# Optimization experiments

Hardware: AMD Instinct MI355X
Metric: run time of the kernel (lower is better)

The kernel has to match this reference:

```python
import jax, jax.numpy as jnp
import numpy as np

KSIZE = 3  # module init kwarg


def setup_inputs() -> dict:
    key = jax.random.key(0)
    k1, k2, k3 = jax.random.split(key, 3)
    shape = (16, 3, 512, 512)  # [B, C, H, W]
    return {
        "sr": jax.random.normal(k1, shape, jnp.float32),
        "sr_ema": jax.random.normal(k2, shape, jnp.float32),
        "hr": jax.random.normal(k3, shape, jnp.float32),
    }


def _local_var(res, ksize):
    """Unbiased variance over a ksize x ksize sliding window with reflect pad.

    Matches torch: reflect-pad then unfold + var(unbiased=True). Implemented as a
    box-filter over sum and sum-of-squares (no ksize^2-larger unfold tensor).
    res: [B, 1, H, W] -> [B, 1, H, W]
    """
    pad = (ksize - 1) // 2
    rp = jnp.pad(res, ((0, 0), (0, 0), (pad, pad), (pad, pad)), mode="reflect")
    n = ksize * ksize
    win = (1, 1, ksize, ksize)
    strides = (1, 1, 1, 1)
    zero = jnp.zeros((), rp.dtype)
    s = jax.lax.reduce_window(rp, zero, jax.lax.add, win, strides, "VALID")
    sq = jax.lax.reduce_window(rp * rp, zero, jax.lax.add, win, strides, "VALID")
    # unbiased: (sum(x^2) - sum(x)^2/n) / (n-1)
    return (sq - s * s / n) / (n - 1)


def reference(sr, sr_ema, hr):
    # per-pixel channel-summed residuals, [B, 1, H, W]
    residual_ema = jnp.sum(jnp.abs(hr - sr_ema), axis=1, keepdims=True) / 255.0
    residual_sr = jnp.sum(jnp.abs(hr - sr), axis=1, keepdims=True) / 255.0

    r_det = jax.lax.stop_gradient(residual_sr)  # .clone().detach() in torch

    # patch-level weight: unbiased var over (C=1, H, W) per sample, ** (1/5)
    n_patch = r_det.shape[1] * r_det.shape[2] * r_det.shape[3]
    mean = jnp.mean(r_det, axis=(-1, -2, -3), keepdims=True)
    patch_var = jnp.sum((r_det - mean) ** 2, axis=(-1, -2, -3), keepdims=True) / (n_patch - 1)
    patch_w = patch_var ** 0.2  # [B,1,1,1]

    pixel_w = _local_var(r_det, KSIZE)  # [B,1,H,W]

    overall_w = patch_w * pixel_w
    overall_w = jnp.where(residual_sr < residual_ema, jnp.zeros((), overall_w.dtype), overall_w)

    # L1 loss (mean reduction) between weighted sr and weighted hr
    return jnp.mean(jnp.abs(overall_w * sr - overall_w * hr))
```

## Files before the change

### kernel.cpp

```cpp
#include <hip/hip_runtime.h>
#include <math.h>


#define BB 16
#define HH 512
#define WW 512
#define HW (HH * WW)
#define CHW (3 * HW)
#define TILES_PER_BATCH 64
#define NBLOCKS (BB * TILES_PER_BATCH)
#define LDS_STRIDE 264

__device__ __forceinline__ int reflect_h(int gh) {
  gh = gh < 0 ? -gh : gh;
  return gh >= HH ? 2 * HH - 2 - gh : gh;
}

__global__ __launch_bounds__(256) void wl1_main(
    const float* __restrict__ sr, const float* __restrict__ srema,
    const float* __restrict__ hr,
    float* __restrict__ p_sum, float* __restrict__ p_sum2,
    float* __restrict__ p_loss) {
  __shared__ float rt[18][LDS_STRIDE];
  const int bid = blockIdx.x;
  const int b = bid >> 6;
  const int t = bid & 63;
  const int h0 = (t >> 1) << 4;
  const int w0 = (t & 1) << 8;
  const int tid = threadIdx.x;
  const int c4 = tid & 63;
  const int rs = tid >> 6;
  const float* __restrict__ srb = sr + (size_t)b * CHW;
  const float* __restrict__ hrb = hr + (size_t)b * CHW;
  const float* __restrict__ eb = srema + (size_t)b * CHW;

#pragma unroll
  for (int it = 0; it < 5; ++it) {
    int row = it * 4 + rs;
    if (row < 18) {
      int gh = reflect_h(h0 - 1 + row);
      const float* hb = hrb + gh * WW + w0 + 4 * c4;
      const float* sb = srb + gh * WW + w0 + 4 * c4;
      float4 ha = *(const float4*)(hb);
      float4 hbv = *(const float4*)(hb + HW);
      float4 hc = *(const float4*)(hb + 2 * HW);
      float4 sa = *(const float4*)(sb);
      float4 sbv = *(const float4*)(sb + HW);
      float4 sc = *(const float4*)(sb + 2 * HW);
      float4 r4;
      r4.x = (fabsf(ha.x - sa.x) + fabsf(hbv.x - sbv.x) + fabsf(hc.x - sc.x)) / 255.0f;
      r4.y = (fabsf(ha.y - sa.y) + fabsf(hbv.y - sbv.y) + fabsf(hc.y - sc.y)) / 255.0f;
      r4.z = (fabsf(ha.z - sa.z) + fabsf(hbv.z - sbv.z) + fabsf(hc.z - sc.z)) / 255.0f;
      r4.w = (fabsf(ha.w - sa.w) + fabsf(hbv.w - sbv.w) + fabsf(hc.w - sc.w)) / 255.0f;
      *(float4*)&rt[row][4 + 4 * c4] = r4;
    }
  }
  if (tid < 36) {
    int row = tid >> 1, side = tid & 1;
    int gh = reflect_h(h0 - 1 + row);
    int gw = side ? w0 + 256 : w0 - 1;
    if (gw < 0) gw = 1;
    if (gw > 511) gw = 1022 - gw;
    int base = gh * WW + gw;
    float v = (fabsf(hrb[base] - srb[base]) +
               fabsf(hrb[base + HW] - srb[base + HW]) +
               fabsf(hrb[base + 2 * HW] - srb[base + 2 * HW])) /
              255.0f;
    rt[row][side ? 260 : 3] = v;
  }
  __syncthreads();

  float v1 = 0.f, v2 = 0.f, v3 = 0.f;
  const int row0 = rs * 4;
#pragma unroll
  for (int rr = 0; rr < 4; ++rr) {
    const int orow = row0 + rr;
    float cs[6] = {0, 0, 0, 0, 0, 0}, cq[6] = {0, 0, 0, 0, 0, 0};
    float center[4];
#pragma unroll
    for (int dr = 0; dr < 3; ++dr) {
      const float* lp = &rt[orow + dr][4 * c4];
      float4 a = *(const float4*)(lp);
      float4 bq = *(const float4*)(lp + 4);
      float4 cq4 = *(const float4*)(lp + 8);
      float f3 = a.w, f4 = bq.x, f5 = bq.y, f6 = bq.z, f7 = bq.w, f8 = cq4.x;
      cs[0] += f3; cq[0] += f3 * f3;
      cs[1] += f4; cq[1] += f4 * f4;
      cs[2] += f5; cq[2] += f5 * f5;
      cs[3] += f6; cq[3] += f6 * f6;
      cs[4] += f7; cq[4] += f7 * f7;
      cs[5] += f8; cq[5] += f8 * f8;
      if (dr == 1) { center[0] = f4; center[1] = f5; center[2] = f6; center[3] = f7; }
    }
    const int gbase = (h0 + orow) * WW + w0 + 4 * c4;
    float4 ha = *(const float4*)(hrb + gbase);
    float4 hb2 = *(const float4*)(hrb + gbase + HW);
    float4 hc = *(const float4*)(hrb + gbase + 2 * HW);
    float4 ea = *(const float4*)(eb + gbase);
    float4 eb2 = *(const float4*)(eb + gbase + HW);
    float4 ec = *(const float4*)(eb + gbase + 2 * HW);
    float e4[4];
    e4[0] = (fabsf(ha.x - ea.x) + fabsf(hb2.x - eb2.x) + fabsf(hc.x - ec.x)) / 255.0f;
    e4[1] = (fabsf(ha.y - ea.y) + fabsf(hb2.y - eb2.y) + fabsf(hc.y - ec.y)) / 255.0f;
    e4[2] = (fabsf(ha.z - ea.z) + fabsf(hb2.z - eb2.z) + fabsf(hc.z - ec.z)) / 255.0f;
    e4[3] = (fabsf(ha.w - ea.w) + fabsf(hb2.w - eb2.w) + fabsf(hc.w - ec.w)) / 255.0f;
#pragma unroll
    for (int cc = 0; cc < 4; ++cc) {
      float s = cs[cc] + cs[cc + 1] + cs[cc + 2];
      float q = cq[cc] + cq[cc + 1] + cq[cc + 2];
      float pvar = (q - s * s / 9.0f) / 8.0f;
      float rc = center[cc];
      v1 += rc;
      v2 += rc * rc;
      if (rc >= e4[cc]) v3 += pvar * (255.0f * rc);
    }
  }

#pragma unroll
  for (int off = 32; off > 0; off >>= 1) {
    v1 += __shfl_down(v1, off, 64);
    v2 += __shfl_down(v2, off, 64);
    v3 += __shfl_down(v3, off, 64);
  }
  __shared__ float red[3][4];
  if (c4 == 0) {
    red[0][rs] = v1;
    red[1][rs] = v2;
    red[2][rs] = v3;
  }
  __syncthreads();
  if (tid == 0) {
    p_sum[bid] = red[0][0] + red[0][1] + red[0][2] + red[0][3];
    p_sum2[bid] = red[1][0] + red[1][1] + red[1][2] + red[1][3];
    p_loss[bid] = red[2][0] + red[2][1] + red[2][2] + red[2][3];
  }
}

__global__ __launch_bounds__(1024) void wl1_reduce(
    const float* __restrict__ p_sum, const float* __restrict__ p_sum2,
    const float* __restrict__ p_loss, float* __restrict__ out) {
  const int tid = threadIdx.x;
  const int b = tid >> 6, k = tid & 63;
  const int i = b * TILES_PER_BATCH + k;
  double s = (double)p_sum[i], s2 = (double)p_sum2[i], sl = (double)p_loss[i];
#pragma unroll
  for (int off = 32; off > 0; off >>= 1) {
    s += __shfl_down(s, off, 64);
    s2 += __shfl_down(s2, off, 64);
    sl += __shfl_down(sl, off, 64);
  }
  __shared__ double acc[BB];
  if (k == 0) {
    const double n = (double)HW;
    double var = (s2 - s * s / n) / (n - 1.0);
    acc[b] = pow(var, 0.2) * sl;
  }
  __syncthreads();
  if (tid == 0) {
    double tot = 0.0;
#pragma unroll
    for (int j = 0; j < BB; ++j) tot += acc[j];
    out[0] = (float)(tot / (double)((size_t)BB * CHW));
  }
}

extern "C" void kernel_launch(void* const* d_in, const int* in_sizes, int n_in,
                              void* d_out, int out_size, void* d_ws,
                              size_t ws_size, hipStream_t stream) {
  const float* sr = (const float*)d_in[0];
  const float* srema = (const float*)d_in[1];
  const float* hr = (const float*)d_in[2];
  float* out = (float*)d_out;

  float* p_sum = (float*)d_ws;
  float* p_sum2 = p_sum + NBLOCKS;
  float* p_loss = p_sum2 + NBLOCKS;

  wl1_main<<<NBLOCKS, 256, 0, stream>>>(sr, srema, hr, p_sum, p_sum2, p_loss);
  wl1_reduce<<<1, 1024, 0, stream>>>(p_sum, p_sum2, p_loss, out);
}
```

Baseline: 158.8 us.

## Halve tile width and compute EMA residual from staged hr loads

Tiles shrink from 256 to 128 columns, which doubles the block count and raises the occupancy hint to 8 blocks per CU. Each thread computes the sr_ema residual in the load phase, reusing the hr float4 values already fetched for the sr residual. This removes the second read of hr in the compute loop. The reduce kernel now folds two partials per thread to cover the 128 tiles per batch. The extra halo traffic from narrower tiles and the conditional register selection are the trade-offs.

After: 166.4 us. +4.8%, slower.

```diff
diff --git a/kernel.cpp b/kernel.cpp
--- a/kernel.cpp
+++ b/kernel.cpp
@@ -7,38 +7,42 @@
 #define WW 512
 #define HW (HH * WW)
 #define CHW (3 * HW)
-#define TILES_PER_BATCH 64
+#define TILE_W 128
+#define TILES_PER_BATCH 128
 #define NBLOCKS (BB * TILES_PER_BATCH)
-#define LDS_STRIDE 264
+#define LDS_STRIDE 136
 
 __device__ __forceinline__ int reflect_h(int gh) {
   gh = gh < 0 ? -gh : gh;
   return gh >= HH ? 2 * HH - 2 - gh : gh;
 }
 
-__global__ __launch_bounds__(256) void wl1_main(
+__global__ __launch_bounds__(256, 8) void wl1_main(
     const float* __restrict__ sr, const float* __restrict__ srema,
     const float* __restrict__ hr,
     float* __restrict__ p_sum, float* __restrict__ p_sum2,
     float* __restrict__ p_loss) {
   __shared__ float rt[18][LDS_STRIDE];
   const int bid = blockIdx.x;
-  const int b = bid >> 6;
-  const int t = bid & 63;
-  const int h0 = (t >> 1) << 4;
-  const int w0 = (t & 1) << 8;
+  const int b = bid >> 7;
+  const int t = bid & 127;
+  const int h0 = (t >> 2) << 4;
+  const int w0 = (t & 3) << 7;
   const int tid = threadIdx.x;
-  const int c4 = tid & 63;
-  const int rs = tid >> 6;
+  const int c4 = tid & 31;
+  const int rsub = tid >> 5;
+  const int ob = (rsub + 7) & 7;
   const float* __restrict__ srb = sr + (size_t)b * CHW;
   const float* __restrict__ hrb = hr + (size_t)b * CHW;
   const float* __restrict__ eb = srema + (size_t)b * CHW;
 
+  float e0[4] = {0.f, 0.f, 0.f, 0.f};
+  float e1[4] = {0.f, 0.f, 0.f, 0.f};
 #pragma unroll
-  for (int it = 0; it < 5; ++it) {
-    int row = it * 4 + rs;
+  for (int it = 0; it < 3; ++it) {
+    const int row = it * 8 + rsub;
     if (row < 18) {
-      int gh = reflect_h(h0 - 1 + row);
+      const int gh = reflect_h(h0 - 1 + row);
       const float* hb = hrb + gh * WW + w0 + 4 * c4;
       const float* sb = srb + gh * WW + w0 + 4 * c4;
       float4 ha = *(const float4*)(hb);
@@ -53,12 +57,28 @@
       r4.z = (fabsf(ha.z - sa.z) + fabsf(hbv.z - sbv.z) + fabsf(hc.z - sc.z)) / 255.0f;
       r4.w = (fabsf(ha.w - sa.w) + fabsf(hbv.w - sbv.w) + fabsf(hc.w - sc.w)) / 255.0f;
       *(float4*)&rt[row][4 + 4 * c4] = r4;
+      const int orow = row - 1;
+      if (orow >= 0 && orow < 16) {
+        const float* ep = eb + gh * WW + w0 + 4 * c4;
+        float4 ea = *(const float4*)(ep);
+        float4 eb2 = *(const float4*)(ep + HW);
+        float4 ec = *(const float4*)(ep + 2 * HW);
+        float ex = (fabsf(ha.x - ea.x) + fabsf(hbv.x - eb2.x) + fabsf(hc.x - ec.x)) / 255.0f;
+        float ey = (fabsf(ha.y - ea.y) + fabsf(hbv.y - eb2.y) + fabsf(hc.y - ec.y)) / 255.0f;
+        float ez = (fabsf(ha.z - ea.z) + fabsf(hbv.z - eb2.z) + fabsf(hc.z - ec.z)) / 255.0f;
+        float ew = (fabsf(ha.w - ea.w) + fabsf(hbv.w - eb2.w) + fabsf(hc.w - ec.w)) / 255.0f;
+        if (orow == ob) {
+          e0[0] = ex; e0[1] = ey; e0[2] = ez; e0[3] = ew;
+        } else {
+          e1[0] = ex; e1[1] = ey; e1[2] = ez; e1[3] = ew;
+        }
+      }
     }
   }
   if (tid < 36) {
     int row = tid >> 1, side = tid & 1;
     int gh = reflect_h(h0 - 1 + row);
-    int gw = side ? w0 + 256 : w0 - 1;
+    int gw = side ? w0 + TILE_W : w0 - 1;
     if (gw < 0) gw = 1;
     if (gw > 511) gw = 1022 - gw;
     int base = gh * WW + gw;
@@ -66,15 +86,14 @@
                fabsf(hrb[base + HW] - srb[base + HW]) +
                fabsf(hrb[base + 2 * HW] - srb[base + 2 * HW])) /
               255.0f;
-    rt[row][side ? 260 : 3] = v;
+    rt[row][side ? 4 + TILE_W : 3] = v;
   }
   __syncthreads();
 
   float v1 = 0.f, v2 = 0.f, v3 = 0.f;
-  const int row0 = rs * 4;
 #pragma unroll
-  for (int rr = 0; rr < 4; ++rr) {
-    const int orow = row0 + rr;
+  for (int rr = 0; rr < 2; ++rr) {
+    const int orow = ob + rr * 8;
     float cs[6] = {0, 0, 0, 0, 0, 0}, cq[6] = {0, 0, 0, 0, 0, 0};
     float center[4];
 #pragma unroll
@@ -92,18 +111,7 @@
       cs[5] += f8; cq[5] += f8 * f8;
       if (dr == 1) { center[0] = f4; center[1] = f5; center[2] = f6; center[3] = f7; }
     }
-    const int gbase = (h0 + orow) * WW + w0 + 4 * c4;
-    float4 ha = *(const float4*)(hrb + gbase);
-    float4 hb2 = *(const float4*)(hrb + gbase + HW);
-    float4 hc = *(const float4*)(hrb + gbase + 2 * HW);
-    float4 ea = *(const float4*)(eb + gbase);
-    float4 eb2 = *(const float4*)(eb + gbase + HW);
-    float4 ec = *(const float4*)(eb + gbase + 2 * HW);
-    float e4[4];
-    e4[0] = (fabsf(ha.x - ea.x) + fabsf(hb2.x - eb2.x) + fabsf(hc.x - ec.x)) / 255.0f;
-    e4[1] = (fabsf(ha.y - ea.y) + fabsf(hb2.y - eb2.y) + fabsf(hc.y - ec.y)) / 255.0f;
-    e4[2] = (fabsf(ha.z - ea.z) + fabsf(hb2.z - eb2.z) + fabsf(hc.z - ec.z)) / 255.0f;
-    e4[3] = (fabsf(ha.w - ea.w) + fabsf(hb2.w - eb2.w) + fabsf(hc.w - ec.w)) / 255.0f;
+    const float* e4 = rr ? e1 : e0;
 #pragma unroll
     for (int cc = 0; cc < 4; ++cc) {
       float s = cs[cc] + cs[cc + 1] + cs[cc + 2];
@@ -123,10 +131,11 @@
     v3 += __shfl_down(v3, off, 64);
   }
   __shared__ float red[3][4];
-  if (c4 == 0) {
-    red[0][rs] = v1;
-    red[1][rs] = v2;
-    red[2][rs] = v3;
+  const int wv = tid >> 6;
+  if ((tid & 63) == 0) {
+    red[0][wv] = v1;
+    red[1][wv] = v2;
+    red[2][wv] = v3;
   }
   __syncthreads();
   if (tid == 0) {
@@ -142,7 +151,9 @@
   const int tid = threadIdx.x;
   const int b = tid >> 6, k = tid & 63;
   const int i = b * TILES_PER_BATCH + k;
-  double s = (double)p_sum[i], s2 = (double)p_sum2[i], sl = (double)p_loss[i];
+  double s = (double)p_sum[i] + (double)p_sum[i + 64];
+  double s2 = (double)p_sum2[i] + (double)p_sum2[i + 64];
+  double sl = (double)p_loss[i] + (double)p_loss[i + 64];
 #pragma unroll
   for (int off = 32; off > 0; off >>= 1) {
     s += __shfl_down(s, off, 64);
```
